# Optimization experiments

Hardware: AMD Instinct MI355X
Metric: run time of the kernel (lower is better)

The kernel has to match this reference:

```python
import jax, jax.numpy as jnp
import numpy as np


def setup_inputs() -> dict:
    key = jax.random.key(0)
    ks = jax.random.split(key, 7)
    b, c, t, h, w = 2, 64, 8, 32, 32
    d = 64
    return {
        "video_features": jax.random.normal(ks[0], (b, c, t, h, w), dtype=jnp.float32),
        "wq": jax.random.normal(ks[1], (d, c), dtype=jnp.float32) * 0.05,
        "bq": jax.random.normal(ks[2], (d,), dtype=jnp.float32) * 0.05,
        "wk": jax.random.normal(ks[3], (d, c), dtype=jnp.float32) * 0.05,
        "bk": jax.random.normal(ks[4], (d,), dtype=jnp.float32) * 0.05,
        "wv": jax.random.normal(ks[5], (d, c), dtype=jnp.float32) * 0.05,
        "bv": jax.random.normal(ks[6], (d,), dtype=jnp.float32) * 0.05,
    }


def reference(video_features, wq, bq, wk, bk, wv, bv):
    b, c, t, h, w = video_features.shape
    d = wq.shape[0]
    xf = video_features.reshape(b, c, t * h * w)  # [b, c, N]
    # 1x1x1 Conv3d == channel-wise linear projection
    q = jnp.einsum('dc,bcn->bnd', wq, xf) + bq                 # [b, N, d]
    k = jnp.einsum('dc,bcn->bnd', wk, xf) + bk                 # [b, N, d]
    v = jnp.einsum('dc,bcn->bnd', wv, xf) + bv                 # [b, N, d]
    scores = jnp.einsum('bnd,bmd->bnm', q, k) / jnp.sqrt(jnp.asarray(d, xf.dtype))  # [b, N, N]
    attn = jax.nn.softmax(scores, axis=-1)
    out = jnp.einsum('bnm,bmd->bnd', attn, v)                  # [b, N, d]
    out = out.transpose(0, 2, 1).reshape(b, d, t, h, w)
    out = out.sum(axis=2).reshape(b, d, 1, h, w)
    return out
```

## Files before the change

kernel.cpp:

```cpp
#include <hip/hip_runtime.h>
#include <math.h>

#define B 2
#define D 64
#define N 8192
#define T 8
#define HW 1024
#define NCH 8
#define KPC (N / NCH)
#define KT 64
#define NT (KPC / KT)
#define QT 256
#define NQT (N / QT)
#define PTS 18

#define LOG2E 1.44269504f

typedef _Float16 half8 __attribute__((ext_vector_type(8)));
typedef _Float16 half4 __attribute__((ext_vector_type(4)));
typedef _Float16 half2 __attribute__((ext_vector_type(2)));
typedef float floatx4 __attribute__((ext_vector_type(4)));

__global__ __launch_bounds__(256)
void proj_kernel(const float* __restrict__ x,
                 const float* __restrict__ wq, const float* __restrict__ bq,
                 const float* __restrict__ wk, const float* __restrict__ bk,
                 const float* __restrict__ wv, const float* __restrict__ bv,
                 _Float16* __restrict__ Qh, _Float16* __restrict__ Kh,
                 _Float16* __restrict__ VTh) {
    int n  = blockIdx.x * 256 + threadIdx.x;
    int d0 = blockIdx.y * 4;
    int b  = blockIdx.z;

    float xcol[64];
    const float* xb = x + (size_t)b * 64 * N + n;
#pragma unroll
    for (int c = 0; c < 64; ++c) xcol[c] = xb[(size_t)c * N];

    float aq[4], ak[4], av[4];
#pragma unroll
    for (int i = 0; i < 4; ++i) { aq[i] = bq[d0+i]; ak[i] = bk[d0+i]; av[i] = bv[d0+i]; }
#pragma unroll
    for (int c = 0; c < 64; ++c) {
        float xv = xcol[c];
#pragma unroll
        for (int i = 0; i < 4; ++i) {
            aq[i] += wq[(d0 + i) * 64 + c] * xv;
            ak[i] += wk[(d0 + i) * 64 + c] * xv;
            av[i] += wv[(d0 + i) * 64 + c] * xv;
        }
    }
    size_t rowb = ((size_t)b * N + n) * 64 + d0;
    half4 hq, hk;
    const float qs = 0.125f * LOG2E;
#pragma unroll
    for (int i = 0; i < 4; ++i) {
        hq[i] = (_Float16)(aq[i] * qs);
        hk[i] = (_Float16)ak[i];
    }
    *(half4*)(Qh + rowb) = hq;
    *(half4*)(Kh + rowb) = hk;
#pragma unroll
    for (int i = 0; i < 4; ++i)
        VTh[((size_t)b * 64 + d0 + i) * N + n] = (_Float16)av[i];
}

__global__ __launch_bounds__(256, 2)
void attn_kernel(const _Float16* __restrict__ Qh, const _Float16* __restrict__ Kh,
                 const _Float16* __restrict__ VTh,
                 _Float16* __restrict__ Opart, float* __restrict__ lpart) {
    __shared__ _Float16 Ks[2][64][72];
    __shared__ _Float16 VTs[2][64][72];

    int bid = blockIdx.x;
    int b   = bid / (NCH * NQT);
    int rem = bid % (NCH * NQT);
    int ch  = rem / NQT;
    int qt  = rem % NQT;
    int q0  = qt * QT;
    int kbase = ch * KPC;

    int tid  = threadIdx.x;
    int wave = tid >> 6;
    int lane = tid & 63;
    int L    = lane & 15;
    int quad = lane >> 4;

    half8 qa[4][2];
#pragma unroll
    for (int g = 0; g < 4; ++g) {
        const _Float16* qrow = Qh + ((size_t)b * N + q0 + wave * 64 + g * 16 + L) * 64;
        qa[g][0] = *(const half8*)(qrow + quad * 8);
        qa[g][1] = *(const half8*)(qrow + 32 + quad * 8);
    }

    floatx4 o[4][4];
    floatx4 lacc[4];
#pragma unroll
    for (int g = 0; g < 4; ++g) {
        lacc[g] = (floatx4)0.f;
#pragma unroll
        for (int s = 0; s < 4; ++s) o[g][s] = (floatx4)0.f;
    }

    half8 ones;
    {
        _Float16 v = (L == 0) ? (_Float16)1.0f : (_Float16)0.0f;
#pragma unroll
        for (int i = 0; i < 8; ++i) ones[i] = v;
    }

    int srow = tid >> 2, sseg = tid & 3;
    const _Float16* Kg = Kh  + (size_t)b * N * 64 + (size_t)sseg * 16;
    const _Float16* Vg = VTh + ((size_t)b * 64 + srow) * N + sseg * 16;

    half8 kr0, kr1, vr0, vr1;
    {
        const _Float16* kp = Kg + (size_t)(kbase + srow) * 64;
        kr0 = *(const half8*)(kp);
        kr1 = *(const half8*)(kp + 8);
        const _Float16* vp = Vg + kbase;
        vr0 = *(const half8*)(vp);
        vr1 = *(const half8*)(vp + 8);
    }
    *(half8*)(&Ks[0][srow][sseg * 16])      = kr0;
    *(half8*)(&Ks[0][srow][sseg * 16 + 8])  = kr1;
    *(half8*)(&VTs[0][srow][sseg * 16])     = vr0;
    *(half8*)(&VTs[0][srow][sseg * 16 + 8]) = vr1;
    __syncthreads();

    for (int kt = 0; kt < NT; ++kt) {
        int cur = kt & 1, nxt = cur ^ 1;
        bool more = (kt + 1 < NT);

        if (more) {
            int kb = kbase + (kt + 1) * KT;
            const _Float16* kp = Kg + (size_t)(kb + srow) * 64;
            kr0 = *(const half8*)(kp);
            kr1 = *(const half8*)(kp + 8);
            const _Float16* vp = Vg + kb;
            vr0 = *(const half8*)(vp);
            vr1 = *(const half8*)(vp + 8);
        }

        half8 kf[4][2], vb[4][2];
#pragma unroll
        for (int sub = 0; sub < 4; ++sub) {
            kf[sub][0] = *(const half8*)(&Ks[cur][sub * 16 + L][quad * 8]);
            kf[sub][1] = *(const half8*)(&Ks[cur][sub * 16 + L][32 + quad * 8]);
            vb[sub][0] = *(const half8*)(&VTs[cur][sub * 16 + L][quad * 8]);
            vb[sub][1] = *(const half8*)(&VTs[cur][sub * 16 + L][32 + quad * 8]);
        }

        _Float16* P0 = &Ks[nxt][wave * 16][0];
        _Float16* P1 = &VTs[nxt][wave * 16][0];

#pragma unroll
        for (int p = 0; p < 2; ++p) {
            floatx4 s[2][4];
#pragma unroll
            for (int sub = 0; sub < 4; ++sub) {
#pragma unroll
                for (int gg = 0; gg < 2; ++gg) {
                    int g = 2 * p + gg;
                    floatx4 acc = (floatx4)0.f;
                    acc = __builtin_amdgcn_mfma_f32_16x16x32_f16(qa[g][0], kf[sub][0], acc, 0, 0, 0);
                    acc = __builtin_amdgcn_mfma_f32_16x16x32_f16(qa[g][1], kf[sub][1], acc, 0, 0, 0);
                    s[gg][sub] = acc;
                }
            }

#pragma unroll
            for (int gg = 0; gg < 2; ++gg)
#pragma unroll
                for (int sub = 0; sub < 4; ++sub)
#pragma unroll
                    for (int r = 0; r < 4; ++r)
                        s[gg][sub][r] = __builtin_amdgcn_exp2f(s[gg][sub][r]);

#pragma unroll
            for (int gg = 0; gg < 2; ++gg) {
                _Float16* Pb = gg ? P1 : P0;
#pragma unroll
                for (int sub = 0; sub < 4; ++sub) {
                    int cb = (sub * 16 + L) * PTS + quad * 4;
                    half2 w0 = {(_Float16)s[gg][sub][0], (_Float16)s[gg][sub][1]};
                    half2 w1 = {(_Float16)s[gg][sub][2], (_Float16)s[gg][sub][3]};
                    *(half2*)(&Pb[cb])     = w0;
                    *(half2*)(&Pb[cb + 2]) = w1;
                }
            }
            half8 pa[2][2];
#pragma unroll
            for (int gg = 0; gg < 2; ++gg) {
                const _Float16* Pb = gg ? P1 : P0;
#pragma unroll
                for (int h = 0; h < 2; ++h) {
                    half8 a;
#pragma unroll
                    for (int j = 0; j < 8; ++j)
                        a[j] = Pb[(h * 32 + quad * 8 + j) * PTS + L];
                    pa[gg][h] = a;
                }
            }

#pragma unroll
            for (int sub = 0; sub < 4; ++sub) {
#pragma unroll
                for (int gg = 0; gg < 2; ++gg) {
                    int g = 2 * p + gg;
                    o[g][sub] = __builtin_amdgcn_mfma_f32_16x16x32_f16(pa[gg][0], vb[sub][0], o[g][sub], 0, 0, 0);
                    o[g][sub] = __builtin_amdgcn_mfma_f32_16x16x32_f16(pa[gg][1], vb[sub][1], o[g][sub], 0, 0, 0);
                }
            }
#pragma unroll
            for (int gg = 0; gg < 2; ++gg) {
                int g = 2 * p + gg;
                lacc[g] = __builtin_amdgcn_mfma_f32_16x16x32_f16(pa[gg][0], ones, lacc[g], 0, 0, 0);
                lacc[g] = __builtin_amdgcn_mfma_f32_16x16x32_f16(pa[gg][1], ones, lacc[g], 0, 0, 0);
            }
        }

        if (more) {
            *(half8*)(&Ks[nxt][srow][sseg * 16])      = kr0;
            *(half8*)(&Ks[nxt][srow][sseg * 16 + 8])  = kr1;
            *(half8*)(&VTs[nxt][srow][sseg * 16])     = vr0;
            *(half8*)(&VTs[nxt][srow][sseg * 16 + 8]) = vr1;
        }
        __syncthreads();
    }

    size_t pb = (size_t)(b * NCH + ch) * N + q0 + wave * 64;
#pragma unroll
    for (int g = 0; g < 4; ++g)
#pragma unroll
        for (int sub = 0; sub < 4; ++sub)
#pragma unroll
            for (int r = 0; r < 4; ++r)
                Opart[(pb + g * 16 + quad * 4 + r) * 64 + sub * 16 + L] =
                    (_Float16)o[g][sub][r];
    if (L == 0) {
#pragma unroll
        for (int g = 0; g < 4; ++g)
#pragma unroll
            for (int r = 0; r < 4; ++r)
                lpart[pb + g * 16 + quad * 4 + r] = lacc[g][r];
    }
}

__global__ void reduce_kernel(const _Float16* __restrict__ Opart,
                              const float* __restrict__ lpart,
                              float* __restrict__ out) {
    int g  = blockIdx.x * 256 + threadIdx.x;
    int d  = g & 63;
    int hw = (g >> 6) & (HW - 1);
    int b  = g >> 16;

    float acc = 0.f;
    for (int t = 0; t < T; ++t) {
        int row = t * HW + hw;
        float Lsum = 0.f, num = 0.f;
#pragma unroll
        for (int c = 0; c < NCH; ++c) {
            size_t pb = (size_t)(b * NCH + c) * N + row;
            Lsum += lpart[pb];
            num  += (float)Opart[pb * 64 + d];
        }
        acc += num / Lsum;
    }
    out[((size_t)b * D + d) * HW + hw] = acc;
}

extern "C" void kernel_launch(void* const* d_in, const int* in_sizes, int n_in,
                              void* d_out, int out_size, void* d_ws, size_t ws_size,
                              hipStream_t stream) {
    const float* x  = (const float*)d_in[0];
    const float* wq = (const float*)d_in[1];
    const float* bq = (const float*)d_in[2];
    const float* wk = (const float*)d_in[3];
    const float* bk = (const float*)d_in[4];
    const float* wv = (const float*)d_in[5];
    const float* bv = (const float*)d_in[6];

    const size_t QSZ = (size_t)B * N * 64;
    _Float16* Qh    = (_Float16*)d_ws;
    _Float16* Kh    = Qh + QSZ;
    _Float16* VTh   = Kh + QSZ;
    _Float16* Opart = VTh + QSZ;
    float*    lpart = (float*)(Opart + (size_t)B * NCH * N * 64);

    proj_kernel<<<dim3(N / 256, 16, B), 256, 0, stream>>>(x, wq, bq, wk, bk, wv, bv,
                                                          Qh, Kh, VTh);
    attn_kernel<<<B * NCH * NQT, 256, 0, stream>>>(Qh, Kh, VTh, Opart, lpart);
    reduce_kernel<<<(B * HW * D) / 256, 256, 0, stream>>>(Opart, lpart, (float*)d_out);
}
```

Before: 137.4 us.

## Transpose score MFMA and redistribute P via permlane swaps instead of LDS

Swaps the operand order of the QK^T MFMA so each lane holds scores in a transposed layout. The probabilities are packed to fp16 with cvt_pkrtz, then rearranged into the A-operand layout for the PV MFMA using permlane32/16 swaps, which avoids the LDS write/read round-trip and the strided scalar LDS gathers. A fallback path keeps an LDS staging buffer, now with a contiguous row stride and vector loads. The risk is that the lane mapping must exactly match the MFMA operand layout, and permlane support depends on the gfx950 compiler.

Result: faster. 127.9 us (-6.9%).

```diff
diff --git a/kernel.cpp b/kernel.cpp
--- a/kernel.cpp
+++ b/kernel.cpp
@@ -12,7 +12,6 @@
 #define NT (KPC / KT)
 #define QT 256
 #define NQT (N / QT)
-#define PTS 18
 
 #define LOG2E 1.44269504f
 
@@ -20,6 +19,7 @@
 typedef _Float16 half4 __attribute__((ext_vector_type(4)));
 typedef _Float16 half2 __attribute__((ext_vector_type(2)));
 typedef float floatx4 __attribute__((ext_vector_type(4)));
+typedef unsigned uint2v __attribute__((ext_vector_type(2)));
 
 __global__ __launch_bounds__(256)
 void proj_kernel(const float* __restrict__ x,
@@ -152,8 +152,10 @@
             vb[sub][1] = *(const half8*)(&VTs[cur][sub * 16 + L][32 + quad * 8]);
         }
 
+#if !__has_builtin(__builtin_amdgcn_permlane32_swap) || !__has_builtin(__builtin_amdgcn_permlane16_swap)
         _Float16* P0 = &Ks[nxt][wave * 16][0];
         _Float16* P1 = &VTs[nxt][wave * 16][0];
+#endif
 
 #pragma unroll
         for (int p = 0; p < 2; ++p) {
@@ -164,8 +166,8 @@
                 for (int gg = 0; gg < 2; ++gg) {
                     int g = 2 * p + gg;
                     floatx4 acc = (floatx4)0.f;
-                    acc = __builtin_amdgcn_mfma_f32_16x16x32_f16(qa[g][0], kf[sub][0], acc, 0, 0, 0);
-                    acc = __builtin_amdgcn_mfma_f32_16x16x32_f16(qa[g][1], kf[sub][1], acc, 0, 0, 0);
+                    acc = __builtin_amdgcn_mfma_f32_16x16x32_f16(kf[sub][0], qa[g][0], acc, 0, 0, 0);
+                    acc = __builtin_amdgcn_mfma_f32_16x16x32_f16(kf[sub][1], qa[g][1], acc, 0, 0, 0);
                     s[gg][sub] = acc;
                 }
             }
@@ -178,30 +180,45 @@
                     for (int r = 0; r < 4; ++r)
                         s[gg][sub][r] = __builtin_amdgcn_exp2f(s[gg][sub][r]);
 
+            half8 pa[2][2];
 #pragma unroll
             for (int gg = 0; gg < 2; ++gg) {
-                _Float16* Pb = gg ? P1 : P0;
+                unsigned ph[4][2];
 #pragma unroll
                 for (int sub = 0; sub < 4; ++sub) {
-                    int cb = (sub * 16 + L) * PTS + quad * 4;
-                    half2 w0 = {(_Float16)s[gg][sub][0], (_Float16)s[gg][sub][1]};
-                    half2 w1 = {(_Float16)s[gg][sub][2], (_Float16)s[gg][sub][3]};
-                    *(half2*)(&Pb[cb])     = w0;
-                    *(half2*)(&Pb[cb + 2]) = w1;
-                }
-            }
-            half8 pa[2][2];
-#pragma unroll
-            for (int gg = 0; gg < 2; ++gg) {
-                const _Float16* Pb = gg ? P1 : P0;
+                    auto p0 = __builtin_amdgcn_cvt_pkrtz(s[gg][sub][0], s[gg][sub][1]);
+                    auto p1 = __builtin_amdgcn_cvt_pkrtz(s[gg][sub][2], s[gg][sub][3]);
+                    ph[sub][0] = __builtin_bit_cast(unsigned, p0);
+                    ph[sub][1] = __builtin_bit_cast(unsigned, p1);
+                }
+#if __has_builtin(__builtin_amdgcn_permlane32_swap) && __has_builtin(__builtin_amdgcn_permlane16_swap)
 #pragma unroll
                 for (int h = 0; h < 2; ++h) {
-                    half8 a;
-#pragma unroll
-                    for (int j = 0; j < 8; ++j)
-                        a[j] = Pb[(h * 32 + quad * 8 + j) * PTS + L];
-                    pa[gg][h] = a;
-                }
+                    uint2v s0 = __builtin_amdgcn_permlane32_swap(ph[2 * h][0], ph[2 * h + 1][0], false, false);
+                    uint2v r0 = __builtin_amdgcn_permlane16_swap(s0[0], s0[1], false, false);
+                    uint2v s1 = __builtin_amdgcn_permlane32_swap(ph[2 * h][1], ph[2 * h + 1][1], false, false);
+                    uint2v r1 = __builtin_amdgcn_permlane16_swap(s1[0], s1[1], false, false);
+                    union { half8 v; unsigned w[4]; } u;
+                    u.w[0] = r0[0];
+                    u.w[1] = r1[0];
+                    u.w[2] = r0[1];
+                    u.w[3] = r1[1];
+                    pa[gg][h] = u.v;
+                }
+#else
+                {
+                    _Float16* Pb = gg ? P1 : P0;
+#pragma unroll
+                    for (int sub = 0; sub < 4; ++sub) {
+                        int cb = L * 72 + sub * 16 + quad * 4;
+                        *(unsigned*)(&Pb[cb])     = ph[sub][0];
+                        *(unsigned*)(&Pb[cb + 2]) = ph[sub][1];
+                    }
+#pragma unroll
+                    for (int h = 0; h < 2; ++h)
+                        pa[gg][h] = *(const half8*)(&Pb[L * 72 + h * 32 + quad * 8]);
+                }
+#endif
             }
 
 #pragma unroll
```
